# Performance work log

Hardware: AMD Instinct MI355X
Metric: run time of the kernel (lower is better)

Reference implementation:

```python
import jax, jax.numpy as jnp
import numpy as np

N_NODES = 100000
IN_CH, HIDDEN, OUT_CH = 128, 128, 64
N_POS, N_NEG = 600000, 600000


def _glorot(key, shape):
    lim = float(np.sqrt(6.0 / (shape[0] + shape[1])))
    return jax.random.uniform(key, shape, jnp.float32, -lim, lim)


def setup_inputs() -> dict:
    key = jax.random.key(0)
    k = jax.random.split(key, 7)
    x = jax.random.normal(k[0], (N_NODES, IN_CH), jnp.float32)
    pos_edge_index = jax.random.randint(k[1], (2, N_POS), 0, N_NODES, jnp.int64)
    neg_edge_index = jax.random.randint(k[2], (2, N_NEG), 0, N_NODES, jnp.int64)
    W1 = _glorot(k[3], (IN_CH, HIDDEN))
    b1 = jnp.zeros((HIDDEN,), jnp.float32)
    W2 = _glorot(k[4], (HIDDEN, OUT_CH))
    b2 = jnp.zeros((OUT_CH,), jnp.float32)
    return {"x": x, "pos_edge_index": pos_edge_index, "neg_edge_index": neg_edge_index,
            "W1": W1, "b1": b1, "W2": W2, "b2": b2}


def gcn_conv(x, W, b, src, dst, n_nodes):
    # PyG GCNConv: add self-loops, symmetric deg^-1/2 normalization, linear, bias
    h = x @ W                                               # [N, F_out]
    ones = jnp.ones(src.shape, h.dtype)
    deg = jax.ops.segment_sum(ones, dst, num_segments=n_nodes) + 1.0  # self-loop
    dinv = jax.lax.rsqrt(deg)                               # deg^-0.5, deg >= 1
    norm = dinv[src] * dinv[dst]                            # per-edge norm
    agg = jax.ops.segment_sum(h[src] * norm[:, None], dst, num_segments=n_nodes)
    agg = agg + h * (dinv * dinv)[:, None]                  # self-loop messages
    return agg + b


def reference(x, pos_edge_index, neg_edge_index, W1, b1, W2, b2):
    n = x.shape[0]
    src, dst = pos_edge_index[0], pos_edge_index[1]
    z = gcn_conv(x, W1, b1, src, dst, n)
    z = jax.nn.relu(z)
    z = gcn_conv(z, W2, b2, src, dst, n)
    # decode: gather endpoints of pos+neg edges, elementwise product, sum over feat
    ei = jnp.concatenate([pos_edge_index, neg_edge_index], axis=-1)  # [2, E_pos+E_neg]
    return jnp.sum(z[ei[0]] * z[ei[1]], axis=-1)
```

## Files before the change

kernel.cpp:

```cpp
#include <hip/hip_runtime.h>

#define N_NODES 100000
#define IN_CH 128
#define HIDDEN 128
#define OUT_CH 64
#define N_POS 600000
#define N_NEG 600000

typedef unsigned int uint32;
typedef unsigned short ushort16;
typedef __attribute__((ext_vector_type(8))) short bf16x8;
typedef __attribute__((ext_vector_type(4))) float f32x4;

__device__ inline float bf_lo(uint32 u) {
    union { uint32 i; float f; } v;
    v.i = u << 16;
    return v.f;
}
__device__ inline float bf_hi(uint32 u) {
    union { uint32 i; float f; } v;
    v.i = u & 0xffff0000u;
    return v.f;
}
__device__ inline ushort16 f2bf(float f) {
    union { uint32 i; float f; } v;
    v.f = f;
    uint32 r = v.i + 0x7fffu + ((v.i >> 16) & 1u);
    return (ushort16)(r >> 16);
}
__device__ inline uint32 pack2bf(float a, float b) {
    return (uint32)f2bf(a) | ((uint32)f2bf(b) << 16);
}

#define NB_HIST ((N_POS + 255) / 256)
#define NB_FILL ((N_POS + 255) / 256)
#define NB_GEMM1 ((N_NODES + 63) / 64)
#define NB_ZERO ((N_NODES + 255) / 256)
#define NB_HG_GROUPS ((NB_HIST + 2) / 3)
#define NB_HG (NB_HG_GROUPS * 5)

__global__ void init_wt(int* __restrict__ hist,
                        const float* __restrict__ W1, const float* __restrict__ W2,
                        ushort16* __restrict__ W1t, ushort16* __restrict__ W2t) {
    if (blockIdx.x < NB_ZERO) {
        int i = blockIdx.x * 256 + threadIdx.x;
        if (i < N_NODES) hist[i] = 0;
    } else {
        int i = (blockIdx.x - NB_ZERO) * 256 + threadIdx.x;
        if (i < 128 * 128) {
            int n = i >> 7, k = i & 127;
            W1t[i] = f2bf(W1[k * 128 + n]);
        } else {
            int j = i - 128 * 128;
            if (j < 64 * 128) {
                int n = j >> 7, k = j & 127;
                W2t[j] = f2bf(W2[k * 64 + n]);
            }
        }
    }
}

__device__ __forceinline__ void gemm_tile(const float* __restrict__ X,
                                          const ushort16* __restrict__ Wt,
                                          ushort16* __restrict__ H, int n, int tileIdx) {
    constexpr int K = 128;
    constexpr int TN = 64;
    constexpr int KH = 32;
    constexpr int XS = 40;
    __shared__ __align__(16) short pool[(TN + 128) * XS];
    short* Xs = pool;
    short* Ws = pool + TN * XS;
    int tid = threadIdx.x;
    int node0 = tileIdx * TN;

    constexpr int CT = 8;
    int w = tid >> 6;
    int lane = tid & 63;
    int l15 = lane & 15;
    int quad = lane >> 4;
    f32x4 acc[CT] = {};

#pragma unroll
    for (int h = 0; h < 4; ++h) {
        if (h) __syncthreads();
        for (int q = tid; q < 128 * 4; q += 256) {
            int row = q >> 2, c = q & 3;
            uint4 v = *(const uint4*)((const short*)Wt + row * K + h * KH + c * 8);
            *(uint4*)(Ws + row * XS + c * 8) = v;
        }
        {
            int row = tid >> 2, part = tid & 3;
            int gn = node0 + row;
            int kl = part * 8;
            float4 v0 = (gn < n) ? *(const float4*)(X + (size_t)gn * K + h * KH + kl)
                                 : float4{0, 0, 0, 0};
            float4 v1 = (gn < n) ? *(const float4*)(X + (size_t)gn * K + h * KH + kl + 4)
                                 : float4{0, 0, 0, 0};
            uint4 p = {pack2bf(v0.x, v0.y), pack2bf(v0.z, v0.w),
                       pack2bf(v1.x, v1.y), pack2bf(v1.z, v1.w)};
            *(uint4*)(Xs + row * XS + kl) = p;
        }
        __syncthreads();

        bf16x8 a = *(const bf16x8*)(Xs + (w * 16 + l15) * XS + quad * 8);
#pragma unroll
        for (int ct = 0; ct < CT; ++ct) {
            bf16x8 b = *(const bf16x8*)(Ws + (ct * 16 + l15) * XS + quad * 8);
            acc[ct] = __builtin_amdgcn_mfma_f32_16x16x32_bf16(a, b, acc[ct], 0, 0, 0);
        }
    }

    short* TB = pool;
#pragma unroll
    for (int p = 0; p < 2; ++p) {
        __syncthreads();
        if ((w >> 1) == p) {
            int rbase = (w & 1) * 16 + quad * 4;
#pragma unroll
            for (int ct = 0; ct < CT; ++ct) {
#pragma unroll
                for (int r = 0; r < 4; ++r) {
                    TB[(rbase + r) * 136 + ct * 16 + l15] = f2bf(acc[ct][r]);
                }
            }
        }
        __syncthreads();
#pragma unroll
        for (int k = 0; k < 2; ++k) {
            int idx = tid + 256 * k;
            int row = idx >> 4, c = idx & 15;
            int gn = node0 + p * 32 + row;
            if (gn < n) {
                uint4 v = *(const uint4*)(TB + row * 136 + c * 8);
                *(uint4*)((short*)H + (size_t)gn * 128 + c * 8) = v;
            }
        }
    }
}

__global__ __launch_bounds__(256) void hist_gemm(
    const int* __restrict__ dst, int* __restrict__ hist, int* __restrict__ rank,
    const float* __restrict__ x, const ushort16* __restrict__ W1t,
    ushort16* __restrict__ H, int n) {
    int bid = blockIdx.x;
    int g = bid / 5, r = bid % 5;
    if (r < 3) {
        int hb = g * 3 + r;
        if (hb >= NB_HIST) return;
        int i = hb * 256 + threadIdx.x;
        if (i < N_POS) rank[i] = atomicAdd(&hist[dst[i]], 1);
    } else {
        int gb = g * 2 + (r - 3);
        if (gb >= NB_GEMM1) return;
        gemm_tile(x, W1t, H, n, gb);
    }
}

__global__ void scan_reduce(const int* __restrict__ hist, int* __restrict__ partials, int n) {
    __shared__ int sdata[256];
    int b = blockIdx.x, t = threadIdx.x;
    int base = b * 1024;
    int s = 0;
    for (int i = t; i < 1024; i += 256) {
        int idx = base + i;
        s += (idx < n) ? hist[idx] : 0;
    }
    sdata[t] = s;
    __syncthreads();
    for (int off = 128; off > 0; off >>= 1) {
        if (t < off) sdata[t] += sdata[t + off];
        __syncthreads();
    }
    if (t == 0) partials[b] = sdata[0];
}

__global__ void scan_final(const int* __restrict__ hist, const int* __restrict__ partials,
                           int* __restrict__ rowstart, float* __restrict__ dinv, int n) {
    __shared__ int tsum[256];
    __shared__ int base_sh;
    int t = threadIdx.x, b = blockIdx.x;
    if (t < 64) {
        int s0 = (t < b) ? partials[t] : 0;
        int i2 = t + 64;
        int s1 = (i2 < b && i2 < 98) ? partials[i2] : 0;
        int s = s0 + s1;
#pragma unroll
        for (int off = 32; off > 0; off >>= 1) s += __shfl_down(s, off, 64);
        if (t == 0) base_sh = s;
    }
    int base = b * 1024 + t * 4;
    int v[4];
    int s = 0;
#pragma unroll
    for (int j = 0; j < 4; j++) {
        int i = base + j;
        v[j] = (i < n) ? hist[i] : 0;
        s += v[j];
    }
    tsum[t] = s;
    __syncthreads();
    for (int off = 1; off < 256; off <<= 1) {
        int a = (t >= off) ? tsum[t - off] : 0;
        __syncthreads();
        tsum[t] += a;
        __syncthreads();
    }
    int offset = base_sh + (tsum[t] - s);
#pragma unroll
    for (int j = 0; j < 4; j++) {
        int i = base + j;
        if (i < n) {
            rowstart[i] = offset;
            dinv[i] = rsqrtf((float)v[j] + 1.0f);
            offset += v[j];
        }
    }
    if (b == 0 && t == 0) rowstart[n] = N_POS;
}

__global__ __launch_bounds__(256) void csr_fill(
    const int* __restrict__ src, const int* __restrict__ dst, const float* __restrict__ dinv,
    const int* __restrict__ rowstart, const int* __restrict__ rank,
    int2* __restrict__ adjw) {
    int e = blockIdx.x * 256 + threadIdx.x;
    if (e < N_POS) {
        int s = src[e], d = dst[e];
        int p = rowstart[d] + rank[e];
        adjw[p] = int2{s, __float_as_int(dinv[s] * dinv[d])};
    }
}

__device__ __forceinline__ uint4 agg_node128(int node, int l, const int* __restrict__ rowstart,
                                             const int2* __restrict__ adjw,
                                             const float* __restrict__ dinv,
                                             const ushort16* __restrict__ H,
                                             const float* __restrict__ bias) {
    float dn = dinv[node];
    int rs = rowstart[node], re = rowstart[node + 1];
    int deg = re - rs;
    int pc = (deg > 0) ? rs : (rs > 0 ? rs - 1 : 0);
    uint4 h[8];
    float wv[8];
#pragma unroll
    for (int j = 0; j < 8; ++j) {
        int p = (rs + j < re) ? rs + j : pc;
        int2 e = adjw[p];
        h[j] = *(const uint4*)(H + (size_t)e.x * 128 + l * 8);
        wv[j] = (j < deg) ? __int_as_float(e.y) : 0.0f;
    }
    float s0[8] = {}, s1[8] = {};
#pragma unroll
    for (int j = 0; j < 8; j += 2) {
        s0[0] += bf_lo(h[j].x) * wv[j]; s0[1] += bf_hi(h[j].x) * wv[j];
        s0[2] += bf_lo(h[j].y) * wv[j]; s0[3] += bf_hi(h[j].y) * wv[j];
        s0[4] += bf_lo(h[j].z) * wv[j]; s0[5] += bf_hi(h[j].z) * wv[j];
        s0[6] += bf_lo(h[j].w) * wv[j]; s0[7] += bf_hi(h[j].w) * wv[j];
        s1[0] += bf_lo(h[j + 1].x) * wv[j + 1]; s1[1] += bf_hi(h[j + 1].x) * wv[j + 1];
        s1[2] += bf_lo(h[j + 1].y) * wv[j + 1]; s1[3] += bf_hi(h[j + 1].y) * wv[j + 1];
        s1[4] += bf_lo(h[j + 1].z) * wv[j + 1]; s1[5] += bf_hi(h[j + 1].z) * wv[j + 1];
        s1[6] += bf_lo(h[j + 1].w) * wv[j + 1]; s1[7] += bf_hi(h[j + 1].w) * wv[j + 1];
    }
    for (int p = rs + 8; p < re; p += 4) {
        uint4 ht[4];
        float wt[4];
#pragma unroll
        for (int j = 0; j < 4; ++j) {
            int q = (p + j < re) ? p + j : p;
            int2 e = adjw[q];
            ht[j] = *(const uint4*)(H + (size_t)e.x * 128 + l * 8);
            wt[j] = (p + j < re) ? __int_as_float(e.y) : 0.0f;
        }
#pragma unroll
        for (int j = 0; j < 4; j += 2) {
            s0[0] += bf_lo(ht[j].x) * wt[j]; s0[1] += bf_hi(ht[j].x) * wt[j];
            s0[2] += bf_lo(ht[j].y) * wt[j]; s0[3] += bf_hi(ht[j].y) * wt[j];
            s0[4] += bf_lo(ht[j].z) * wt[j]; s0[5] += bf_hi(ht[j].z) * wt[j];
            s0[6] += bf_lo(ht[j].w) * wt[j]; s0[7] += bf_hi(ht[j].w) * wt[j];
            s1[0] += bf_lo(ht[j + 1].x) * wt[j + 1]; s1[1] += bf_hi(ht[j + 1].x) * wt[j + 1];
            s1[2] += bf_lo(ht[j + 1].y) * wt[j + 1]; s1[3] += bf_hi(ht[j + 1].y) * wt[j + 1];
            s1[4] += bf_lo(ht[j + 1].z) * wt[j + 1]; s1[5] += bf_hi(ht[j + 1].z) * wt[j + 1];
            s1[6] += bf_lo(ht[j + 1].w) * wt[j + 1]; s1[7] += bf_hi(ht[j + 1].w) * wt[j + 1];
        }
    }
    uint4 hv = *(const uint4*)(H + (size_t)node * 128 + l * 8);
    float4 bv0 = *(const float4*)(bias + l * 8);
    float4 bv1 = *(const float4*)(bias + l * 8 + 4);
    float d2 = dn * dn;
    float hs[8] = {bf_lo(hv.x), bf_hi(hv.x), bf_lo(hv.y), bf_hi(hv.y),
                   bf_lo(hv.z), bf_hi(hv.z), bf_lo(hv.w), bf_hi(hv.w)};
    float bb[8] = {bv0.x, bv0.y, bv0.z, bv0.w, bv1.x, bv1.y, bv1.z, bv1.w};
    float v[8];
#pragma unroll
    for (int j = 0; j < 8; ++j) {
        v[j] = fmaxf(s0[j] + s1[j] + hs[j] * d2 + bb[j], 0.0f);
    }
    return uint4{pack2bf(v[0], v[1]), pack2bf(v[2], v[3]), pack2bf(v[4], v[5]),
                 pack2bf(v[6], v[7])};
}

#define ZS 136
#define TN2 32
__global__ __launch_bounds__(256, 4) void agg1_gemm2(
    const int* __restrict__ rowstart, const int2* __restrict__ adjw,
    const float* __restrict__ dinv, const ushort16* __restrict__ H,
    const float* __restrict__ b1, const ushort16* __restrict__ W2t,
    ushort16* __restrict__ h2, int n) {
    __shared__ __align__(16) short Zs[TN2 * ZS];
    __shared__ __align__(16) short Ws[64 * ZS];
    int tid = threadIdx.x;
    int node0 = blockIdx.x * TN2;

    for (int q = tid; q < 64 * 16; q += 256) {
        int row = q >> 4, c = q & 15;
        uint4 v = *(const uint4*)((const short*)W2t + row * 128 + c * 8);
        *(uint4*)(Ws + row * ZS + c * 8) = v;
    }

    int g = tid >> 4, l = tid & 15;
#pragma unroll 1
    for (int it = 0; it < 2; ++it) {
        int row = g * 2 + it;
        int node = node0 + row;
        uint4 z = (node < n) ? agg_node128(node, l, rowstart, adjw, dinv, H, b1)
                             : uint4{0, 0, 0, 0};
        *(uint4*)(Zs + row * ZS + l * 8) = z;
    }
    __syncthreads();

    int w = tid >> 6, lane = tid & 63, l15 = lane & 15, quad = lane >> 4;
    int wr = w >> 1, wc = w & 1;
    f32x4 acc[2] = {};
    const short* zrow = Zs + (wr * 16 + l15) * ZS + quad * 8;
#pragma unroll
    for (int kk = 0; kk < 4; ++kk) {
        bf16x8 a = *(const bf16x8*)(zrow + kk * 32);
#pragma unroll
        for (int ct = 0; ct < 2; ++ct) {
            bf16x8 b = *(const bf16x8*)(Ws + (wc * 32 + ct * 16 + l15) * ZS + quad * 8 + kk * 32);
            acc[ct] = __builtin_amdgcn_mfma_f32_16x16x32_bf16(a, b, acc[ct], 0, 0, 0);
        }
    }
#pragma unroll
    for (int ct = 0; ct < 2; ++ct) {
#pragma unroll
        for (int r = 0; r < 4; ++r) {
            int gn = node0 + wr * 16 + quad * 4 + r;
            if (gn < n) h2[(size_t)gn * OUT_CH + wc * 32 + ct * 16 + l15] = f2bf(acc[ct][r]);
        }
    }
}

__global__ void agg_pull64(const int* __restrict__ rowstart, const int2* __restrict__ adjw,
                           const float* __restrict__ dinv, const ushort16* __restrict__ H,
                           const float* __restrict__ bias, ushort16* __restrict__ Z, int n) {
    int g = threadIdx.x >> 4;
    int l = threadIdx.x & 15;
    int nodeA = blockIdx.x * 32 + g * 2;
    if (nodeA >= n) return;
    int nodeB = nodeA + 1;
    bool hasB = nodeB < n;
    int nB = hasB ? nodeB : nodeA;
    float dnA = dinv[nodeA], dnB = dinv[nB];
    int rsA = rowstart[nodeA], reA = rowstart[nodeA + 1];
    int rsB = rowstart[nB], reB = rowstart[nB + 1];
    int degA = reA - rsA, degB = reB - rsB;
    int pcA = (degA > 0) ? rsA : (rsA > 0 ? rsA - 1 : 0);
    int pcB = (degB > 0) ? rsB : (rsB > 0 ? rsB - 1 : 0);
    uint2 hA[8], hB[8];
    float wA[8], wB[8];
#pragma unroll
    for (int j = 0; j < 8; ++j) {
        int2 ea = adjw[(rsA + j < reA) ? rsA + j : pcA];
        int2 eb = adjw[(rsB + j < reB) ? rsB + j : pcB];
        hA[j] = *(const uint2*)(H + (size_t)ea.x * 64 + l * 4);
        hB[j] = *(const uint2*)(H + (size_t)eb.x * 64 + l * 4);
        wA[j] = (j < degA) ? __int_as_float(ea.y) : 0.0f;
        wB[j] = (j < degB) ? __int_as_float(eb.y) : 0.0f;
    }
    float sA[4] = {}, sB[4] = {};
#pragma unroll
    for (int j = 0; j < 8; ++j) {
        sA[0] += bf_lo(hA[j].x) * wA[j]; sA[1] += bf_hi(hA[j].x) * wA[j];
        sA[2] += bf_lo(hA[j].y) * wA[j]; sA[3] += bf_hi(hA[j].y) * wA[j];
        sB[0] += bf_lo(hB[j].x) * wB[j]; sB[1] += bf_hi(hB[j].x) * wB[j];
        sB[2] += bf_lo(hB[j].y) * wB[j]; sB[3] += bf_hi(hB[j].y) * wB[j];
    }
    for (int p = rsA + 8; p < reA; p += 4) {
        uint2 ht[4];
        float wt[4];
#pragma unroll
        for (int j = 0; j < 4; ++j) {
            int q = (p + j < reA) ? p + j : p;
            int2 e = adjw[q];
            ht[j] = *(const uint2*)(H + (size_t)e.x * 64 + l * 4);
            wt[j] = (p + j < reA) ? __int_as_float(e.y) : 0.0f;
        }
#pragma unroll
        for (int j = 0; j < 4; ++j) {
            sA[0] += bf_lo(ht[j].x) * wt[j]; sA[1] += bf_hi(ht[j].x) * wt[j];
            sA[2] += bf_lo(ht[j].y) * wt[j]; sA[3] += bf_hi(ht[j].y) * wt[j];
        }
    }
    for (int p = rsB + 8; p < reB; p += 4) {
        uint2 ht[4];
        float wt[4];
#pragma unroll
        for (int j = 0; j < 4; ++j) {
            int q = (p + j < reB) ? p + j : p;
            int2 e = adjw[q];
            ht[j] = *(const uint2*)(H + (size_t)e.x * 64 + l * 4);
            wt[j] = (p + j < reB) ? __int_as_float(e.y) : 0.0f;
        }
#pragma unroll
        for (int j = 0; j < 4; ++j) {
            sB[0] += bf_lo(ht[j].x) * wt[j]; sB[1] += bf_hi(ht[j].x) * wt[j];
            sB[2] += bf_lo(ht[j].y) * wt[j]; sB[3] += bf_hi(ht[j].y) * wt[j];
        }
    }
    uint2 hvA = *(const uint2*)(H + (size_t)nodeA * 64 + l * 4);
    uint2 hvB = *(const uint2*)(H + (size_t)nB * 64 + l * 4);
    float4 bv = *(const float4*)(bias + l * 4);
    float d2A = dnA * dnA, d2B = dnB * dnB;
    float bb[4] = {bv.x, bv.y, bv.z, bv.w};
    float hsA[4] = {bf_lo(hvA.x), bf_hi(hvA.x), bf_lo(hvA.y), bf_hi(hvA.y)};
    float hsB[4] = {bf_lo(hvB.x), bf_hi(hvB.x), bf_lo(hvB.y), bf_hi(hvB.y)};
    float vA[4], vB[4];
#pragma unroll
    for (int j = 0; j < 4; ++j) {
        vA[j] = sA[j] + hsA[j] * d2A + bb[j];
        vB[j] = sB[j] + hsB[j] * d2B + bb[j];
    }
    *(uint2*)(Z + (size_t)nodeA * 64 + l * 4) = uint2{pack2bf(vA[0], vA[1]), pack2bf(vA[2], vA[3])};
    if (hasB)
        *(uint2*)(Z + (size_t)nodeB * 64 + l * 4) =
            uint2{pack2bf(vB[0], vB[1]), pack2bf(vB[2], vB[3])};
}

__global__ void decode_mfma(const int* __restrict__ pos, const int* __restrict__ neg,
                            const short* __restrict__ Z, float* __restrict__ out) {
    int wid = threadIdx.x >> 6;
    int lane = threadIdx.x & 63;
    int l15 = lane & 15;
    int quad = lane >> 4;
    int e0 = (blockIdx.x * 4 + wid) * 32;
    if (e0 >= N_POS + N_NEG) return;
    const int* bp = (e0 < N_POS) ? pos : (neg - N_POS);
    int eA = e0 + l15;
    int eB = e0 + 16 + l15;
    int aA = bp[eA], bA = bp[600000 + eA];
    int aB = bp[eB], bB = bp[600000 + eB];

    const short* zaA = Z + (size_t)aA * OUT_CH + quad * 8;
    const short* zbA = Z + (size_t)bA * OUT_CH + quad * 8;
    const short* zaB = Z + (size_t)aB * OUT_CH + quad * 8;
    const short* zbB = Z + (size_t)bB * OUT_CH + quad * 8;
    bf16x8 a0A = *(const bf16x8*)(zaA);
    bf16x8 a1A = *(const bf16x8*)(zaA + 32);
    bf16x8 b0A = *(const bf16x8*)(zbA);
    bf16x8 b1A = *(const bf16x8*)(zbA + 32);
    bf16x8 a0B = *(const bf16x8*)(zaB);
    bf16x8 a1B = *(const bf16x8*)(zaB + 32);
    bf16x8 b0B = *(const bf16x8*)(zbB);
    bf16x8 b1B = *(const bf16x8*)(zbB + 32);

    f32x4 accA = {}, accB = {};
    accA = __builtin_amdgcn_mfma_f32_16x16x32_bf16(a0A, b0A, accA, 0, 0, 0);
    accB = __builtin_amdgcn_mfma_f32_16x16x32_bf16(a0B, b0B, accB, 0, 0, 0);
    accA = __builtin_amdgcn_mfma_f32_16x16x32_bf16(a1A, b1A, accA, 0, 0, 0);
    accB = __builtin_amdgcn_mfma_f32_16x16x32_bf16(a1B, b1B, accB, 0, 0, 0);

    if (quad == (l15 >> 2)) {
        out[eA] = accA[l15 & 3];
        out[eB] = accB[l15 & 3];
    }
}

extern "C" void kernel_launch(void* const* d_in, const int* in_sizes, int n_in,
                              void* d_out, int out_size, void* d_ws, size_t ws_size,
                              hipStream_t stream) {
    const float* x = (const float*)d_in[0];
    const int* pos = (const int*)d_in[1];
    const int* neg = (const int*)d_in[2];
    const float* W1 = (const float*)d_in[3];
    const float* b1 = (const float*)d_in[4];
    const float* W2 = (const float*)d_in[5];
    const float* b2 = (const float*)d_in[6];
    float* out = (float*)d_out;

    ushort16* A = (ushort16*)d_ws;
    ushort16* B = A + (size_t)N_NODES * 128;
    float* dinv = (float*)(B + (size_t)N_NODES * 128);
    int* hist = (int*)(dinv + N_NODES);
    int* rowstart = hist + N_NODES;
    int2* adjw = (int2*)(rowstart + N_NODES + 1);
    int* partials = (int*)(adjw + N_POS);
    ushort16* W1t = (ushort16*)(partials + 128);
    ushort16* W2t = W1t + 128 * 128;
    int* rank = (int*)B;

    const int* pos_src = pos;
    const int* pos_dst = pos + N_POS;

    constexpr int NB_SCAN = (N_NODES + 1023) / 1024;

    init_wt<<<NB_ZERO + 96, 256, 0, stream>>>(hist, W1, W2, W1t, W2t);

    hist_gemm<<<NB_HG, 256, 0, stream>>>(pos_dst, hist, rank, x, W1t, A, N_NODES);

    scan_reduce<<<NB_SCAN, 256, 0, stream>>>(hist, partials, N_NODES);
    scan_final<<<NB_SCAN, 256, 0, stream>>>(hist, partials, rowstart, dinv, N_NODES);

    csr_fill<<<NB_FILL, 256, 0, stream>>>(pos_src, pos_dst, dinv, rowstart, rank, adjw);

    agg1_gemm2<<<(N_NODES + TN2 - 1) / TN2, 256, 0, stream>>>(rowstart, adjw, dinv, A, b1, W2t,
                                                              B, N_NODES);

    agg_pull64<<<(N_NODES + 31) / 32, 256, 0, stream>>>(rowstart, adjw, dinv, B, b2, A, N_NODES);

    decode_mfma<<<(N_POS + N_NEG) / 128, 256, 0, stream>>>(pos, neg, (const short*)A, out);
}
```

Baseline: 243.7 us.

## Add intra-block dynamic work stealing for node aggregation in both GCN layers

Both aggregation kernels now hand out node chunks to warps dynamically through a shared-memory atomic counter, instead of a fixed node-to-warp mapping, to even out load imbalance from varying node degrees. agg_pull64 also doubles its nodes per block, halving the grid, and its body moves into a device helper. This adds an extra barrier, atomics and shuffles per chunk, and the larger blocks give fewer of them to spread across CUs.

```diff
diff --git a/kernel.cpp b/kernel.cpp
--- a/kernel.cpp
+++ b/kernel.cpp
@@ -307,8 +307,11 @@
     ushort16* __restrict__ h2, int n) {
     __shared__ __align__(16) short Zs[TN2 * ZS];
     __shared__ __align__(16) short Ws[64 * ZS];
+    __shared__ int next4;
     int tid = threadIdx.x;
     int node0 = blockIdx.x * TN2;
+    if (tid == 0) next4 = 4;
+    __syncthreads();
 
     for (int q = tid; q < 64 * 16; q += 256) {
         int row = q >> 4, c = q & 15;
@@ -317,17 +320,23 @@
     }
 
     int g = tid >> 4, l = tid & 15;
-#pragma unroll 1
-    for (int it = 0; it < 2; ++it) {
-        int row = g * 2 + it;
+    int w = tid >> 6, lane = tid & 63;
+    int sub = g & 3;
+    int chunk = w;
+    while (chunk < TN2 / 4) {
+        int row = chunk * 4 + sub;
         int node = node0 + row;
         uint4 z = (node < n) ? agg_node128(node, l, rowstart, adjw, dinv, H, b1)
                              : uint4{0, 0, 0, 0};
         *(uint4*)(Zs + row * ZS + l * 8) = z;
+        int nc;
+        if (lane == 0) nc = atomicAdd(&next4, 1);
+        nc = __shfl(nc, 0, 64);
+        chunk = nc;
     }
     __syncthreads();
 
-    int w = tid >> 6, lane = tid & 63, l15 = lane & 15, quad = lane >> 4;
+    int l15 = lane & 15, quad = lane >> 4;
     int wr = w >> 1, wc = w & 1;
     f32x4 acc[2] = {};
     const short* zrow = Zs + (wr * 16 + l15) * ZS + quad * 8;
@@ -350,13 +359,13 @@
     }
 }
 
-__global__ void agg_pull64(const int* __restrict__ rowstart, const int2* __restrict__ adjw,
-                           const float* __restrict__ dinv, const ushort16* __restrict__ H,
-                           const float* __restrict__ bias, ushort16* __restrict__ Z, int n) {
-    int g = threadIdx.x >> 4;
-    int l = threadIdx.x & 15;
-    int nodeA = blockIdx.x * 32 + g * 2;
-    if (nodeA >= n) return;
+__device__ __forceinline__ void agg_pair64(int nodeA, int n, int l,
+                                           const int* __restrict__ rowstart,
+                                           const int2* __restrict__ adjw,
+                                           const float* __restrict__ dinv,
+                                           const ushort16* __restrict__ H,
+                                           const float* __restrict__ bias,
+                                           ushort16* __restrict__ Z) {
     int nodeB = nodeA + 1;
     bool hasB = nodeB < n;
     int nB = hasB ? nodeB : nodeA;
@@ -434,6 +443,29 @@
     if (hasB)
         *(uint2*)(Z + (size_t)nodeB * 64 + l * 4) =
             uint2{pack2bf(vB[0], vB[1]), pack2bf(vB[2], vB[3])};
+}
+
+__global__ void agg_pull64(const int* __restrict__ rowstart, const int2* __restrict__ adjw,
+                           const float* __restrict__ dinv, const ushort16* __restrict__ H,
+                           const float* __restrict__ bias, ushort16* __restrict__ Z, int n) {
+    __shared__ int next4;
+    int tid = threadIdx.x;
+    if (tid == 0) next4 = 4;
+    __syncthreads();
+    int g = tid >> 4, l = tid & 15;
+    int w = tid >> 6, lane = tid & 63;
+    int sub = g & 3;
+    int base = blockIdx.x * 64;
+    int chunk = w;
+    while (chunk < 8) {
+        int pr = chunk * 4 + sub;
+        int nodeA = base + pr * 2;
+        if (nodeA < n) agg_pair64(nodeA, n, l, rowstart, adjw, dinv, H, bias, Z);
+        int nc;
+        if (lane == 0) nc = atomicAdd(&next4, 1);
+        nc = __shfl(nc, 0, 64);
+        chunk = nc;
+    }
 }
 
 __global__ void decode_mfma(const int* __restrict__ pos, const int* __restrict__ neg,
@@ -515,7 +547,7 @@
     agg1_gemm2<<<(N_NODES + TN2 - 1) / TN2, 256, 0, stream>>>(rowstart, adjw, dinv, A, b1, W2t,
                                                               B, N_NODES);
 
-    agg_pull64<<<(N_NODES + 31) / 32, 256, 0, stream>>>(rowstart, adjw, dinv, B, b2, A, N_NODES);
+    agg_pull64<<<(N_NODES + 63) / 64, 256, 0, stream>>>(rowstart, adjw, dinv, B, b2, A, N_NODES);
 
     decode_mfma<<<(N_POS + N_NEG) / 128, 256, 0, stream>>>(pos, neg, (const short*)A, out);
 }
```

Measured after the change: 247.5 us. No clear change (+1.6%).
